# Performance work log

Hardware: AMD Instinct MI355X
Metric: run time of the kernel (lower is better)

## Reference

```python
import jax, jax.numpy as jnp
import numpy as np

T, B, I, H = 1024, 32768, 1, 3  # time steps, batch, input size, hidden size (from nn.LSTM(1,3,1,...))


def setup_inputs() -> dict:
    key = jax.random.key(0)
    ks = jax.random.split(key, 7)
    return {
        "x": jax.random.normal(ks[0], (T, B, I), dtype=jnp.float32),
        "h0": jax.random.normal(ks[1], (B, H), dtype=jnp.float32),
        "c0": jax.random.normal(ks[2], (B, H), dtype=jnp.float32),
        "W_ih": jax.random.normal(ks[3], (4 * H, I), dtype=jnp.float32) * (1.0 / np.sqrt(H)),
        "W_hh": jax.random.normal(ks[4], (4 * H, H), dtype=jnp.float32) * (1.0 / np.sqrt(H)),
        "b_ih": jax.random.normal(ks[5], (4 * H,), dtype=jnp.float32) * (1.0 / np.sqrt(H)),
        "b_hh": jax.random.normal(ks[6], (4 * H,), dtype=jnp.float32) * (1.0 / np.sqrt(H)),
    }


def reference(x, h0, c0, W_ih, W_hh, b_ih, b_hh):
    """Sequential single-layer LSTM over T steps (PyTorch gate order i,f,g,o).

    x: [T, B, I]; returns hidden-state sequence ys: [T, B, H].
    """
    # Precompute input projection for all steps at once: [T, B, 4H]
    x_proj = jnp.einsum("tbi,gi->tbg", x, W_ih) + b_ih + b_hh

    def step(carry, xg):
        h, c = carry
        gates = xg + h @ W_hh.T  # [B, 4H]
        i_, f_, g_, o_ = jnp.split(gates, 4, axis=-1)
        c_new = jax.nn.sigmoid(f_) * c + jax.nn.sigmoid(i_) * jnp.tanh(g_)
        h_new = jax.nn.sigmoid(o_) * jnp.tanh(c_new)
        return (h_new, c_new), h_new

    (hn, cn), ys = jax.lax.scan(step, (h0, c0), x_proj)
    return ys
```

## Files before the change

kernel.cpp:

```cpp
#include <hip/hip_runtime.h>


constexpr int T_STEPS = 1024;
constexpr int BATCH   = 32768;
constexpr int HID     = 3;
constexpr int NB      = 16;

__device__ __forceinline__ float fsigmoid(float z) {
    float e = __builtin_amdgcn_exp2f(-1.4426950408889634f * z);
    return __builtin_amdgcn_rcpf(1.0f + e);
}
__device__ __forceinline__ float ftanh(float z) {
    float e = __builtin_amdgcn_exp2f(2.8853900817779268f * z);
    return 1.0f - 2.0f * __builtin_amdgcn_rcpf(e + 1.0f);
}

template <int CTRL>
__device__ __forceinline__ float qbcast(float v) {
    return __int_as_float(
        __builtin_amdgcn_update_dpp(0, __float_as_int(v), CTRL, 0xF, 0xF, true));
}

__global__ __launch_bounds__(256, 2) void lstm_quad_kernel(
    const float* __restrict__ x,
    const float* __restrict__ h0,
    const float* __restrict__ c0,
    const float* __restrict__ W_ih,
    const float* __restrict__ W_hh,
    const float* __restrict__ b_ih,
    const float* __restrict__ b_hh,
    float* __restrict__ out)
{
    const int tid  = blockIdx.x * 256 + threadIdx.x;
    const int lane = tid & 3;
    const int b    = tid >> 2;
    const int u    = (lane == 3) ? 0 : lane;

    float wiv[4], bv[4], w0[4], w1[4], w2[4];
#pragma unroll
    for (int g = 0; g < 4; ++g) {
        const int r = 3 * g + u;
        wiv[g] = W_ih[r];
        bv[g]  = b_ih[r] + b_hh[r];
        w0[g]  = W_hh[r * HID + 0];
        w1[g]  = W_hh[r * HID + 1];
        w2[g]  = W_hh[r * HID + 2];
    }

    float h = h0[b * HID + u];
    float c = c0[b * HID + u];
    const int obase = b * HID + u;

    float cur[NB], nxt[NB];
#pragma unroll
    for (int i = 0; i < NB; ++i) cur[i] = x[i * BATCH + b];

    for (int chunk = 0; chunk < T_STEPS / NB; ++chunk) {
        const int base_next = (chunk + 1) * NB;
#pragma unroll
        for (int i = 0; i < NB; ++i) {
            int tl = base_next + i;
            if (tl >= T_STEPS) tl = T_STEPS - 1;
            nxt[i] = x[tl * BATCH + b];
        }

#pragma unroll
        for (int i = 0; i < NB; ++i) {
            const int t  = chunk * NB + i;
            const float xv = cur[i];

            const float hv0 = qbcast<0x00>(h);
            const float hv1 = qbcast<0x55>(h);
            const float hv2 = qbcast<0xAA>(h);

            float pi = fmaf(xv, wiv[0], bv[0]);
            float pf = fmaf(xv, wiv[1], bv[1]);
            float pg = fmaf(xv, wiv[2], bv[2]);
            float po = fmaf(xv, wiv[3], bv[3]);
            pi = fmaf(hv0, w0[0], pi); pi = fmaf(hv1, w1[0], pi); pi = fmaf(hv2, w2[0], pi);
            pf = fmaf(hv0, w0[1], pf); pf = fmaf(hv1, w1[1], pf); pf = fmaf(hv2, w2[1], pf);
            pg = fmaf(hv0, w0[2], pg); pg = fmaf(hv1, w1[2], pg); pg = fmaf(hv2, w2[2], pg);
            po = fmaf(hv0, w0[3], po); po = fmaf(hv1, w1[3], po); po = fmaf(hv2, w2[3], po);

            const float ig = fsigmoid(pi);
            const float fg = fsigmoid(pf);
            const float gg = ftanh(pg);
            const float og = fsigmoid(po);
            c = fmaf(fg, c, ig * gg);
            h = og * ftanh(c);

            if (lane < 3) out[t * (BATCH * HID) + obase] = h;
        }

#pragma unroll
        for (int i = 0; i < NB; ++i) cur[i] = nxt[i];
    }
}

extern "C" void kernel_launch(void* const* d_in, const int* in_sizes, int n_in,
                              void* d_out, int out_size, void* d_ws, size_t ws_size,
                              hipStream_t stream) {
    const float* x    = (const float*)d_in[0];
    const float* h0   = (const float*)d_in[1];
    const float* c0   = (const float*)d_in[2];
    const float* W_ih = (const float*)d_in[3];
    const float* W_hh = (const float*)d_in[4];
    const float* b_ih = (const float*)d_in[5];
    const float* b_hh = (const float*)d_in[6];
    float* out = (float*)d_out;

    dim3 grid((4 * BATCH) / 256), block(256);
    lstm_quad_kernel<<<grid, block, 0, stream>>>(x, h0, c0, W_ih, W_hh, b_ih, b_hh, out);
}
```

Baseline: 616.3 us.

## Fold activation scales into weights and share one reciprocal across four gates

The exp2 scale factors for sigmoid and tanh are folded into the input weights, recurrent weights and biases, which removes per-step multiplies. The four gate reciprocals are replaced by a single rcp of the product of the four denominators, with each gate recovered by multiplications. This cuts transcendental work on the serial per-step dependency chain. The x prefetch buffers now ping-pong across two chunks instead of being copied each chunk, and the lane<3 store guard is dropped because lane 3 writes the same value to the same address as lane 0. The shared reciprocal can overflow to inf and produce NaN when gate pre-activations are large.

```diff
diff --git a/kernel.cpp b/kernel.cpp
--- a/kernel.cpp
+++ b/kernel.cpp
@@ -6,14 +6,7 @@
 constexpr int HID     = 3;
 constexpr int NB      = 16;
 
-__device__ __forceinline__ float fsigmoid(float z) {
-    float e = __builtin_amdgcn_exp2f(-1.4426950408889634f * z);
-    return __builtin_amdgcn_rcpf(1.0f + e);
-}
-__device__ __forceinline__ float ftanh(float z) {
-    float e = __builtin_amdgcn_exp2f(2.8853900817779268f * z);
-    return 1.0f - 2.0f * __builtin_amdgcn_rcpf(e + 1.0f);
-}
+constexpr float LOG2E = 1.4426950408889634f;
 
 template <int CTRL>
 __device__ __forceinline__ float qbcast(float v) {
@@ -40,33 +33,35 @@
 #pragma unroll
     for (int g = 0; g < 4; ++g) {
         const int r = 3 * g + u;
-        wiv[g] = W_ih[r];
-        bv[g]  = b_ih[r] + b_hh[r];
-        w0[g]  = W_hh[r * HID + 0];
-        w1[g]  = W_hh[r * HID + 1];
-        w2[g]  = W_hh[r * HID + 2];
+        const float s = (g == 2) ? (2.0f * LOG2E) : (-LOG2E);
+        wiv[g] = s * W_ih[r];
+        bv[g]  = s * (b_ih[r] + b_hh[r]);
+        w0[g]  = s * W_hh[r * HID + 0];
+        w1[g]  = s * W_hh[r * HID + 1];
+        w2[g]  = s * W_hh[r * HID + 2];
     }
 
     float h = h0[b * HID + u];
     float c = c0[b * HID + u];
-    const int obase = b * HID + u;
 
-    float cur[NB], nxt[NB];
+    const float* xp = x + b;
+    float*       op = out + b * HID + u;
+
+    float bufA[NB], bufB[NB];
 #pragma unroll
-    for (int i = 0; i < NB; ++i) cur[i] = x[i * BATCH + b];
+    for (int i = 0; i < NB; ++i) bufA[i] = xp[(size_t)i * BATCH];
 
-    for (int chunk = 0; chunk < T_STEPS / NB; ++chunk) {
+    auto run_chunk = [&](int chunk, float (&cur)[NB], float (&nxt)[NB]) {
         const int base_next = (chunk + 1) * NB;
 #pragma unroll
         for (int i = 0; i < NB; ++i) {
             int tl = base_next + i;
             if (tl >= T_STEPS) tl = T_STEPS - 1;
-            nxt[i] = x[tl * BATCH + b];
+            nxt[i] = xp[(size_t)tl * BATCH];
         }
 
 #pragma unroll
         for (int i = 0; i < NB; ++i) {
-            const int t  = chunk * NB + i;
             const float xv = cur[i];
 
             const float hv0 = qbcast<0x00>(h);
@@ -82,18 +77,39 @@
             pg = fmaf(hv0, w0[2], pg); pg = fmaf(hv1, w1[2], pg); pg = fmaf(hv2, w2[2], pg);
             po = fmaf(hv0, w0[3], po); po = fmaf(hv1, w1[3], po); po = fmaf(hv2, w2[3], po);
 
-            const float ig = fsigmoid(pi);
-            const float fg = fsigmoid(pf);
-            const float gg = ftanh(pg);
-            const float og = fsigmoid(po);
+            const float ei = __builtin_amdgcn_exp2f(pi);
+            const float ef = __builtin_amdgcn_exp2f(pf);
+            const float eg = __builtin_amdgcn_exp2f(pg);
+            const float eo = __builtin_amdgcn_exp2f(po);
+            const float di = 1.0f + ei;
+            const float df = 1.0f + ef;
+            const float dg = 1.0f + eg;
+            const float dn = 1.0f + eo;
+
+            const float p  = di * df;
+            const float q  = dg * dn;
+            const float R  = __builtin_amdgcn_rcpf(p * q);
+            const float rp = q * R;
+            const float rq = p * R;
+            const float ig = df * rp;
+            const float fg = di * rp;
+            const float gi = dn * rq;
+            const float og = dg * rq;
+            const float gg = fmaf(-2.0f, gi, 1.0f);
+
             c = fmaf(fg, c, ig * gg);
-            h = og * ftanh(c);
+            const float ec = __builtin_amdgcn_exp2f((2.0f * LOG2E) * c);
+            const float th = 1.0f - 2.0f * __builtin_amdgcn_rcpf(ec + 1.0f);
+            h = og * th;
 
-            if (lane < 3) out[t * (BATCH * HID) + obase] = h;
+            *op = h;
+            op += BATCH * HID;
         }
+    };
 
-#pragma unroll
-        for (int i = 0; i < NB; ++i) cur[i] = nxt[i];
+    for (int cc = 0; cc < T_STEPS / NB; cc += 2) {
+        run_chunk(cc,     bufA, bufB);
+        run_chunk(cc + 1, bufB, bufA);
     }
 }
 
```

After: 603.0 us. 2.2% less time.
